# Optimization experiments

Measured on AMD Instinct MI355X. Metric: run time of the kernel, lower is better.

The kernel has to match this reference:

```python
import jax, jax.numpy as jnp
import numpy as np

TOP_K = 12
OBS_RADIUS = 1.0
DIST_MIN_THRES = 0.8
EPS = 1e-4


def setup_inputs() -> dict:
    key = jax.random.key(0)
    ks = jax.random.split(key, 9)
    N, in_dim = 4096, 4
    c = in_dim + 2  # pairwise diff + eye flag + (dist - thres)
    states = jax.random.normal(ks[0], (N, in_dim), dtype=jnp.float32) * 2.0
    def w(k, o, i):
        return jax.random.normal(k, (o, i), dtype=jnp.float32) * (1.0 / np.sqrt(i))
    return {
        "states": states,
        "W1": w(ks[1], 64, c),  "b1": jnp.zeros((64,), jnp.float32),
        "W2": w(ks[2], 128, 64), "b2": jnp.zeros((128,), jnp.float32),
        "W3": w(ks[3], 64, 128), "b3": jnp.zeros((64,), jnp.float32),
        "W4": w(ks[4], 1, 64),   "b4": jnp.zeros((1,), jnp.float32),
    }


def _conv1x1(h, W, b):
    # h: [N, C_in, L]; 1x1 Conv1d == channel matmul
    return jnp.einsum('oi,nil->nol', W, h) + b[None, :, None]


def reference(states, W1, b1, W2, b2, W3, b3, W4, b4):
    N = states.shape[0]
    # pairwise differences: [N, N, in_dim]
    x = states[:, None, :] - states[None, :, :]
    d_norm = jnp.sqrt(jnp.sum(jnp.square(x[:, :, :2]) + EPS, axis=2))  # [N, N]
    eye = jnp.eye(N, dtype=x.dtype)
    x = jnp.concatenate(
        [x, eye[:, :, None], (d_norm - DIST_MIN_THRES)[:, :, None]], axis=2
    )  # [N, N, c]
    # remove_distant_agents: keep TOP_K nearest neighbors per agent
    dn = jnp.sqrt(jnp.sum(jnp.square(x[:, :, :2]) + EPS, axis=2))  # [N, N]
    _, idx = jax.lax.top_k(-dn, TOP_K)                              # [N, k]
    x = jnp.take_along_axis(x, idx[:, :, None], axis=1)            # [N, k, c]
    dist = jnp.sqrt(jnp.sum(jnp.square(x[:, :, :2]) + EPS, axis=2, keepdims=True))  # [N,k,1]
    k, c = x.shape[1], x.shape[2]
    mask = (dist <= OBS_RADIUS).astype(x.dtype).reshape(-1, 1, k)  # [N,1,k] (reshape, as in source)
    h = x.reshape(-1, c, k)  # faithful: source uses reshape, NOT transpose
    h = jax.nn.relu(_conv1x1(h, W1, b1))
    h = jax.nn.relu(_conv1x1(h, W2, b2))
    h = jax.nn.relu(_conv1x1(h, W3, b3))
    h = _conv1x1(h, W4, b4)  # [N, 1, k]
    h = h * mask
    return h, mask
```

## Files before the change

### kernel.cpp

```cpp
#include <hip/hip_runtime.h>
#include <stdint.h>

#define NAG 4096
#define TOPK 12
#define EPSF 1e-4f
#define NT 512
#define WPB 8
#define NBLK (NAG / WPB)
#define MTOT (NAG * TOPK)

typedef unsigned long long u64;
typedef short short8v __attribute__((ext_vector_type(8)));
typedef float f32x4 __attribute__((ext_vector_type(4)));

__device__ __forceinline__ unsigned short f2bf(float f) {
    union { float f; unsigned u; } v; v.f = f;
    unsigned r = v.u + 0x7FFFu + ((v.u >> 16) & 1u);
    return (unsigned short)(r >> 16);
}

template <int CTRL>
__device__ __forceinline__ void dpp_min_step(unsigned &hi, unsigned &lo) {
    unsigned ohi = (unsigned)__builtin_amdgcn_update_dpp((int)hi, (int)hi, CTRL, 0xf, 0xf, false);
    unsigned olo = (unsigned)__builtin_amdgcn_update_dpp((int)lo, (int)lo, CTRL, 0xf, 0xf, false);
    bool t = (ohi < hi) || (ohi == hi && olo < lo);
    hi = t ? ohi : hi;
    lo = t ? olo : lo;
}

__global__ __launch_bounds__(256)
void cbf_prep(const float* __restrict__ W2, const float* __restrict__ W3,
              unsigned short* __restrict__ Wb) {
    int idx = blockIdx.x * 256 + threadIdx.x;
    float v = (idx < 8192) ? W2[idx] : W3[idx - 8192];
    Wb[idx] = f2bf(v);
}

__global__ __launch_bounds__(NT, 4)
void cbf_fused(const float* __restrict__ states,
               const float* __restrict__ W1, const float* __restrict__ b1,
               const unsigned short* __restrict__ Wb,
               const float* __restrict__ b2, const float* __restrict__ b3,
               const float* __restrict__ W4, const float* __restrict__ b4,
               float* __restrict__ out)
{
    const int t = threadIdx.x;
    const int lane = t & 63;
    const int wv = t >> 6;
    const int i = blockIdx.x * WPB + wv;

    __shared__ float2 s_xy[NAG];
    __shared__ u64 s_surv[WPB][64];
    __shared__ int s_sel[WPB][TOPK];
    __shared__ float s_x[WPB][72];
    __shared__ float s_mask[WPB][TOPK];
    __shared__ __align__(16) unsigned char s_h2[WPB][4096];

#pragma unroll
    for (int u = 0; u < 8; ++u) {
        int r = u * NT + t;
        float4 sr = reinterpret_cast<const float4*>(states)[r];
        s_xy[r] = make_float2(sr.x, sr.y);
    }
    __syncthreads();

    const float2 sif = s_xy[i];
    const float si0 = sif.x, si1 = sif.y;

    unsigned minb = 0xFFFFFFFFu;
    int minj = 0;
#pragma unroll 8
    for (int u = 0; u < 64; ++u) {
        float2 sj = s_xy[u * 64 + lane];
        float dx0 = __fsub_rn(si0, sj.x);
        float dx1 = __fsub_rn(si1, sj.y);
        float d2 = __fadd_rn(__fadd_rn(__fmul_rn(dx0, dx0), EPSF),
                             __fadd_rn(__fmul_rn(dx1, dx1), EPSF));
        unsigned b = __float_as_uint(__fsqrt_rn(d2));
        if (b < minb) { minb = b; minj = u * 64 + lane; }
    }

    unsigned Tb;
    {
        unsigned khi = minb, klo = (unsigned)minj;
        unsigned Tcur = 0;
        for (int r = 0; r < TOPK; ++r) {
            unsigned hi = khi, lo = klo;
            dpp_min_step<0xB1>(hi, lo);
            dpp_min_step<0x4E>(hi, lo);
            dpp_min_step<0x124>(hi, lo);
            dpp_min_step<0x128>(hi, lo);
            dpp_min_step<0x142>(hi, lo);
            dpp_min_step<0x143>(hi, lo);
            unsigned hw = (unsigned)__builtin_amdgcn_readlane((int)hi, 63);
            unsigned lw = (unsigned)__builtin_amdgcn_readlane((int)lo, 63);
            Tcur = hw;
            if (khi == hw && klo == lw) khi = 0xFFFFFFFFu;
        }
        Tb = Tcur;
    }

    int cnt = 0;
#pragma unroll 8
    for (int u = 0; u < 64; ++u) {
        float2 sj = s_xy[u * 64 + lane];
        float dx0 = __fsub_rn(si0, sj.x);
        float dx1 = __fsub_rn(si1, sj.y);
        float d2 = __fadd_rn(__fadd_rn(__fmul_rn(dx0, dx0), EPSF),
                             __fadd_rn(__fmul_rn(dx1, dx1), EPSF));
        unsigned b = __float_as_uint(__fsqrt_rn(d2));
        bool p = (b <= Tb);
        u64 mk = __ballot(p);
        if (p) {
            int pos = cnt + __popcll(mk & ((1ull << lane) - 1ull));
            if (pos < 64)
                s_surv[wv][pos] = ((u64)b << 32) | (unsigned)(u * 64 + lane);
        }
        cnt += __popcll(mk);
    }
    if (cnt > 64) cnt = 64;
    __asm volatile("s_waitcnt lgkmcnt(0)" ::: "memory");
    __builtin_amdgcn_wave_barrier();

    if (lane < cnt) {
        u64 kA = s_surv[wv][lane];
        int rA = 0;
        for (int q = 0; q < cnt; ++q)
            rA += (s_surv[wv][q] < kA) ? 1 : 0;
        if (rA < TOPK) s_sel[wv][rA] = (int)(unsigned)(kA & 0xffffffffull);
    }
    __asm volatile("s_waitcnt lgkmcnt(0)" ::: "memory");
    __builtin_amdgcn_wave_barrier();

    if (lane < TOPK) {
        int j = s_sel[wv][lane];
        const float4 sj = reinterpret_cast<const float4*>(states)[j];
        const float4 si = reinterpret_cast<const float4*>(states)[i];
        float dx0 = __fsub_rn(si.x, sj.x);
        float dx1 = __fsub_rn(si.y, sj.y);
        float dx2 = __fsub_rn(si.z, sj.z);
        float dx3 = __fsub_rn(si.w, sj.w);
        float d2 = __fadd_rn(__fadd_rn(__fmul_rn(dx0, dx0), EPSF),
                             __fadd_rn(__fmul_rn(dx1, dx1), EPSF));
        float dn = __fsqrt_rn(d2);
        s_x[wv][lane * 6 + 0] = dx0;
        s_x[wv][lane * 6 + 1] = dx1;
        s_x[wv][lane * 6 + 2] = dx2;
        s_x[wv][lane * 6 + 3] = dx3;
        s_x[wv][lane * 6 + 4] = (j == i) ? 1.0f : 0.0f;
        s_x[wv][lane * 6 + 5] = __fsub_rn(dn, 0.8f);
        float mk = (dn <= 1.0f) ? 1.0f : 0.0f;
        s_mask[wv][lane] = mk;
        out[MTOT + i * TOPK + lane] = mk;
    }
    __asm volatile("s_waitcnt lgkmcnt(0)" ::: "memory");
    __builtin_amdgcn_wave_barrier();

    const int r16 = lane & 15;
    const int hi = lane >> 4;

    float xc[6];
#pragma unroll
    for (int ch = 0; ch < 6; ++ch)
        xc[ch] = (r16 < TOPK) ? s_x[wv][ch * TOPK + r16] : 0.0f;

    short8v a0, a1;
#pragma unroll
    for (int e = 0; e < 8; ++e) {
        {
            int o = 8 * hi + e;
            const float2* wr = reinterpret_cast<const float2*>(W1 + o * 6);
            float2 w0 = wr[0], w1 = wr[1], w2 = wr[2];
            float acc = b1[o];
            acc = fmaf(w0.x, xc[0], acc);
            acc = fmaf(w0.y, xc[1], acc);
            acc = fmaf(w1.x, xc[2], acc);
            acc = fmaf(w1.y, xc[3], acc);
            acc = fmaf(w2.x, xc[4], acc);
            acc = fmaf(w2.y, xc[5], acc);
            a0[e] = (r16 < TOPK) ? (short)f2bf(fmaxf(acc, 0.0f)) : (short)0;
        }
        {
            int o = 32 + 8 * hi + e;
            const float2* wr = reinterpret_cast<const float2*>(W1 + o * 6);
            float2 w0 = wr[0], w1 = wr[1], w2 = wr[2];
            float acc = b1[o];
            acc = fmaf(w0.x, xc[0], acc);
            acc = fmaf(w0.y, xc[1], acc);
            acc = fmaf(w1.x, xc[2], acc);
            acc = fmaf(w1.y, xc[3], acc);
            acc = fmaf(w2.x, xc[4], acc);
            acc = fmaf(w2.y, xc[5], acc);
            a1[e] = (r16 < TOPK) ? (short)f2bf(fmaxf(acc, 0.0f)) : (short)0;
        }
    }

    unsigned char* lp2 = s_h2[wv];
    const int c = r16;

#pragma unroll
    for (int nt = 0; nt < 8; ++nt) {
        int o = nt * 16 + c;
        short8v bf0 = *(const short8v*)(Wb + o * 64 + 8 * hi);
        short8v bf1 = *(const short8v*)(Wb + o * 64 + 32 + 8 * hi);
        float bb = b2[o];
        f32x4 acc = {bb, bb, bb, bb};
        acc = __builtin_amdgcn_mfma_f32_16x16x32_bf16(a0, bf0, acc, 0, 0, 0);
        acc = __builtin_amdgcn_mfma_f32_16x16x32_bf16(a1, bf1, acc, 0, 0, 0);
#pragma unroll
        for (int e = 0; e < 4; ++e) {
            unsigned short hv = f2bf(fmaxf(acc[e], 0.0f));
            int mr = 4 * hi + e;
            int slot = (2 * nt + (c >> 3)) ^ (mr & 15);
            *(unsigned short*)(lp2 + mr * 256 + slot * 16 + ((2 * c) & 15)) = hv;
        }
    }
    __asm volatile("s_waitcnt lgkmcnt(0)" ::: "memory");
    __builtin_amdgcn_wave_barrier();

    short8v a3[4];
#pragma unroll
    for (int ks = 0; ks < 4; ++ks)
        a3[ks] = *(short8v*)(lp2 + r16 * 256 + (((4 * ks + hi) ^ r16) * 16));
    float h3r[4][4];
#pragma unroll
    for (int nt = 0; nt < 4; ++nt) {
        int o = nt * 16 + c;
        float bb = b3[o];
        f32x4 ac = {bb, bb, bb, bb};
#pragma unroll
        for (int ks = 0; ks < 4; ++ks) {
            short8v bf = *(const short8v*)(Wb + 8192 + o * 128 + ks * 32 + 8 * hi);
            ac = __builtin_amdgcn_mfma_f32_16x16x32_bf16(a3[ks], bf, ac, 0, 0, 0);
        }
#pragma unroll
        for (int e = 0; e < 4; ++e) h3r[nt][e] = fmaxf(ac[e], 0.0f);
    }

    float w4c[4];
#pragma unroll
    for (int nt = 0; nt < 4; ++nt) w4c[nt] = W4[nt * 16 + c];
    float part[4];
#pragma unroll
    for (int e = 0; e < 4; ++e) {
        float p = h3r[0][e] * w4c[0];
        p = fmaf(h3r[1][e], w4c[1], p);
        p = fmaf(h3r[2][e], w4c[2], p);
        p = fmaf(h3r[3][e], w4c[3], p);
        part[e] = p;
    }
#pragma unroll
    for (int off = 1; off <= 8; off <<= 1) {
#pragma unroll
        for (int e = 0; e < 4; ++e)
            part[e] += __shfl_xor(part[e], off, 64);
    }
    if (c == 0) {
        float bb4 = b4[0];
#pragma unroll
        for (int e = 0; e < 4; ++e) {
            int mr = 4 * hi + e;
            if (mr < TOPK)
                out[i * TOPK + mr] = (part[e] + bb4) * s_mask[wv][mr];
        }
    }
}

extern "C" void kernel_launch(void* const* d_in, const int* in_sizes, int n_in,
                              void* d_out, int out_size, void* d_ws, size_t ws_size,
                              hipStream_t stream) {
    const float* states = (const float*)d_in[0];
    const float* W1 = (const float*)d_in[1];
    const float* b1 = (const float*)d_in[2];
    const float* W2 = (const float*)d_in[3];
    const float* b2 = (const float*)d_in[4];
    const float* W3 = (const float*)d_in[5];
    const float* b3 = (const float*)d_in[6];
    const float* W4 = (const float*)d_in[7];
    const float* b4 = (const float*)d_in[8];
    float* out = (float*)d_out;
    unsigned short* Wb = (unsigned short*)d_ws;

    cbf_prep<<<dim3(64), dim3(256), 0, stream>>>(W2, W3, Wb);
    cbf_fused<<<dim3(NBLK), dim3(NT), 0, stream>>>(states, W1, b1, Wb,
                                                   b2, b3, W4, b4, out);
}
```

Measured before the change: 103.1 us.

## Split each agent's distance scan across two waves and halve the h2 staging buffer

Each agent is now handled by two waves, each scanning half of the 4096 candidates. The per-wave local minima are merged in shared memory for the top-k threshold search, and survivors are compacted through a shared atomic counter. Block size doubles to 1024 threads, and the second wave exits before the MLP stage. The layer-2/layer-3 MFMA chain is also reorganised into two halves so the bf16 h2 staging buffer shrinks from 4 KB to 2 KB per agent. The aim is to expose more parallelism in the scan, at the cost of extra block-wide barriers, atomics, and idle waves during the MLP.

```diff
diff --git a/kernel.cpp b/kernel.cpp
--- a/kernel.cpp
+++ b/kernel.cpp
@@ -4,9 +4,9 @@
 #define NAG 4096
 #define TOPK 12
 #define EPSF 1e-4f
-#define NT 512
-#define WPB 8
-#define NBLK (NAG / WPB)
+#define NT 1024
+#define APB 8
+#define NBLK (NAG / APB)
 #define MTOT (NAG * TOPK)
 
 typedef unsigned long long u64;
@@ -36,7 +36,7 @@
     Wb[idx] = f2bf(v);
 }
 
-__global__ __launch_bounds__(NT, 4)
+__global__ __launch_bounds__(NT, 8)
 void cbf_fused(const float* __restrict__ states,
                const float* __restrict__ W1, const float* __restrict__ b1,
                const unsigned short* __restrict__ Wb,
@@ -47,17 +47,24 @@
     const int t = threadIdx.x;
     const int lane = t & 63;
     const int wv = t >> 6;
-    const int i = blockIdx.x * WPB + wv;
+    const int a = wv >> 1;
+    const int p = wv & 1;
+    const int i = blockIdx.x * APB + a;
 
     __shared__ float2 s_xy[NAG];
-    __shared__ u64 s_surv[WPB][64];
-    __shared__ int s_sel[WPB][TOPK];
-    __shared__ float s_x[WPB][72];
-    __shared__ float s_mask[WPB][TOPK];
-    __shared__ __align__(16) unsigned char s_h2[WPB][4096];
-
-#pragma unroll
-    for (int u = 0; u < 8; ++u) {
+    __shared__ u64 s_lmin[APB][128];
+    __shared__ u64 s_surv[APB][64];
+    __shared__ int s_sel[APB][TOPK];
+    __shared__ float s_x[APB][72];
+    __shared__ float s_mask[APB][TOPK];
+    __shared__ unsigned s_cnt[APB];
+    __shared__ unsigned s_T[APB];
+    __shared__ __align__(16) unsigned char s_h2[APB][2048];
+
+    if (t < APB) s_cnt[t] = 0;
+
+#pragma unroll
+    for (int u = 0; u < 4; ++u) {
         int r = u * NT + t;
         float4 sr = reinterpret_cast<const float4*>(states)[r];
         s_xy[r] = make_float2(sr.x, sr.y);
@@ -70,22 +77,35 @@
     unsigned minb = 0xFFFFFFFFu;
     int minj = 0;
 #pragma unroll 8
-    for (int u = 0; u < 64; ++u) {
-        float2 sj = s_xy[u * 64 + lane];
+    for (int u = 0; u < 32; ++u) {
+        int j = (p * 32 + u) * 64 + lane;
+        float2 sj = s_xy[j];
         float dx0 = __fsub_rn(si0, sj.x);
         float dx1 = __fsub_rn(si1, sj.y);
         float d2 = __fadd_rn(__fadd_rn(__fmul_rn(dx0, dx0), EPSF),
                              __fadd_rn(__fmul_rn(dx1, dx1), EPSF));
         unsigned b = __float_as_uint(__fsqrt_rn(d2));
-        if (b < minb) { minb = b; minj = u * 64 + lane; }
-    }
-
-    unsigned Tb;
-    {
-        unsigned khi = minb, klo = (unsigned)minj;
-        unsigned Tcur = 0;
+        if (b < minb) { minb = b; minj = j; }
+    }
+    s_lmin[a][p * 64 + lane] = ((u64)minb << 32) | (unsigned)minj;
+    __syncthreads();
+
+    if (p == 0) {
+        unsigned khi[2], klo[2];
+#pragma unroll
+        for (int q = 0; q < 2; ++q) {
+            u64 kk = s_lmin[a][lane + q * 64];
+            klo[q] = (unsigned)(kk & 0xffffffffull);
+            khi[q] = (unsigned)(kk >> 32);
+        }
+        unsigned Tb = 0;
         for (int r = 0; r < TOPK; ++r) {
-            unsigned hi = khi, lo = klo;
+            unsigned hi = khi[0], lo = klo[0];
+            {
+                bool tk = (khi[1] < hi) || (khi[1] == hi && klo[1] < lo);
+                hi = tk ? khi[1] : hi;
+                lo = tk ? klo[1] : lo;
+            }
             dpp_min_step<0xB1>(hi, lo);
             dpp_min_step<0x4E>(hi, lo);
             dpp_min_step<0x124>(hi, lo);
@@ -94,46 +114,63 @@
             dpp_min_step<0x143>(hi, lo);
             unsigned hw = (unsigned)__builtin_amdgcn_readlane((int)hi, 63);
             unsigned lw = (unsigned)__builtin_amdgcn_readlane((int)lo, 63);
-            Tcur = hw;
-            if (khi == hw && klo == lw) khi = 0xFFFFFFFFu;
-        }
-        Tb = Tcur;
-    }
-
-    int cnt = 0;
+            Tb = hw;
+#pragma unroll
+            for (int q = 0; q < 2; ++q) {
+                bool w = (khi[q] == hw) && (klo[q] == lw);
+                khi[q] = w ? 0xFFFFFFFFu : khi[q];
+            }
+        }
+        if (lane == 0) s_T[a] = Tb;
+    }
+    __syncthreads();
+
+    {
+        unsigned Tb = s_T[a];
 #pragma unroll 8
-    for (int u = 0; u < 64; ++u) {
-        float2 sj = s_xy[u * 64 + lane];
-        float dx0 = __fsub_rn(si0, sj.x);
-        float dx1 = __fsub_rn(si1, sj.y);
-        float d2 = __fadd_rn(__fadd_rn(__fmul_rn(dx0, dx0), EPSF),
-                             __fadd_rn(__fmul_rn(dx1, dx1), EPSF));
-        unsigned b = __float_as_uint(__fsqrt_rn(d2));
-        bool p = (b <= Tb);
-        u64 mk = __ballot(p);
-        if (p) {
-            int pos = cnt + __popcll(mk & ((1ull << lane) - 1ull));
-            if (pos < 64)
-                s_surv[wv][pos] = ((u64)b << 32) | (unsigned)(u * 64 + lane);
-        }
-        cnt += __popcll(mk);
-    }
-    if (cnt > 64) cnt = 64;
+        for (int u = 0; u < 32; ++u) {
+            int j = (p * 32 + u) * 64 + lane;
+            float2 sj = s_xy[j];
+            float dx0 = __fsub_rn(si0, sj.x);
+            float dx1 = __fsub_rn(si1, sj.y);
+            float d2 = __fadd_rn(__fadd_rn(__fmul_rn(dx0, dx0), EPSF),
+                                 __fadd_rn(__fmul_rn(dx1, dx1), EPSF));
+            unsigned b = __float_as_uint(__fsqrt_rn(d2));
+            bool pr = (b <= Tb);
+            u64 mk = __ballot(pr);
+            if (mk != 0ull) {
+                unsigned nsel = (unsigned)__popcll(mk);
+                unsigned base = 0;
+                if (lane == 0) base = atomicAdd(&s_cnt[a], nsel);
+                base = (unsigned)__builtin_amdgcn_readfirstlane((int)base);
+                if (pr) {
+                    int pos = (int)base + __popcll(mk & ((1ull << lane) - 1ull));
+                    if (pos < 64)
+                        s_surv[a][pos] = ((u64)b << 32) | (unsigned)j;
+                }
+            }
+        }
+    }
+    __syncthreads();
+
+    if (p != 0) return;
+
+    {
+        int cnt = (int)s_cnt[a];
+        if (cnt > 64) cnt = 64;
+        if (lane < cnt) {
+            u64 kA = s_surv[a][lane];
+            int rA = 0;
+            for (int q = 0; q < cnt; ++q)
+                rA += (s_surv[a][q] < kA) ? 1 : 0;
+            if (rA < TOPK) s_sel[a][rA] = (int)(unsigned)(kA & 0xffffffffull);
+        }
+    }
     __asm volatile("s_waitcnt lgkmcnt(0)" ::: "memory");
     __builtin_amdgcn_wave_barrier();
 
-    if (lane < cnt) {
-        u64 kA = s_surv[wv][lane];
-        int rA = 0;
-        for (int q = 0; q < cnt; ++q)
-            rA += (s_surv[wv][q] < kA) ? 1 : 0;
-        if (rA < TOPK) s_sel[wv][rA] = (int)(unsigned)(kA & 0xffffffffull);
-    }
-    __asm volatile("s_waitcnt lgkmcnt(0)" ::: "memory");
-    __builtin_amdgcn_wave_barrier();
-
     if (lane < TOPK) {
-        int j = s_sel[wv][lane];
+        int j = s_sel[a][lane];
         const float4 sj = reinterpret_cast<const float4*>(states)[j];
         const float4 si = reinterpret_cast<const float4*>(states)[i];
         float dx0 = __fsub_rn(si.x, sj.x);
@@ -143,14 +180,14 @@
         float d2 = __fadd_rn(__fadd_rn(__fmul_rn(dx0, dx0), EPSF),
                              __fadd_rn(__fmul_rn(dx1, dx1), EPSF));
         float dn = __fsqrt_rn(d2);
-        s_x[wv][lane * 6 + 0] = dx0;
-        s_x[wv][lane * 6 + 1] = dx1;
-        s_x[wv][lane * 6 + 2] = dx2;
-        s_x[wv][lane * 6 + 3] = dx3;
-        s_x[wv][lane * 6 + 4] = (j == i) ? 1.0f : 0.0f;
-        s_x[wv][lane * 6 + 5] = __fsub_rn(dn, 0.8f);
+        s_x[a][lane * 6 + 0] = dx0;
+        s_x[a][lane * 6 + 1] = dx1;
+        s_x[a][lane * 6 + 2] = dx2;
+        s_x[a][lane * 6 + 3] = dx3;
+        s_x[a][lane * 6 + 4] = (j == i) ? 1.0f : 0.0f;
+        s_x[a][lane * 6 + 5] = __fsub_rn(dn, 0.8f);
         float mk = (dn <= 1.0f) ? 1.0f : 0.0f;
-        s_mask[wv][lane] = mk;
+        s_mask[a][lane] = mk;
         out[MTOT + i * TOPK + lane] = mk;
     }
     __asm volatile("s_waitcnt lgkmcnt(0)" ::: "memory");
@@ -158,11 +195,12 @@
 
     const int r16 = lane & 15;
     const int hi = lane >> 4;
+    const int c = r16;
 
     float xc[6];
 #pragma unroll
     for (int ch = 0; ch < 6; ++ch)
-        xc[ch] = (r16 < TOPK) ? s_x[wv][ch * TOPK + r16] : 0.0f;
+        xc[ch] = (r16 < TOPK) ? s_x[a][ch * TOPK + r16] : 0.0f;
 
     short8v a0, a1;
 #pragma unroll
@@ -195,47 +233,60 @@
         }
     }
 
-    unsigned char* lp2 = s_h2[wv];
-    const int c = r16;
-
-#pragma unroll
-    for (int nt = 0; nt < 8; ++nt) {
-        int o = nt * 16 + c;
-        short8v bf0 = *(const short8v*)(Wb + o * 64 + 8 * hi);
-        short8v bf1 = *(const short8v*)(Wb + o * 64 + 32 + 8 * hi);
-        float bb = b2[o];
-        f32x4 acc = {bb, bb, bb, bb};
-        acc = __builtin_amdgcn_mfma_f32_16x16x32_bf16(a0, bf0, acc, 0, 0, 0);
-        acc = __builtin_amdgcn_mfma_f32_16x16x32_bf16(a1, bf1, acc, 0, 0, 0);
-#pragma unroll
-        for (int e = 0; e < 4; ++e) {
-            unsigned short hv = f2bf(fmaxf(acc[e], 0.0f));
-            int mr = 4 * hi + e;
-            int slot = (2 * nt + (c >> 3)) ^ (mr & 15);
-            *(unsigned short*)(lp2 + mr * 256 + slot * 16 + ((2 * c) & 15)) = hv;
-        }
-    }
-    __asm volatile("s_waitcnt lgkmcnt(0)" ::: "memory");
-    __builtin_amdgcn_wave_barrier();
-
-    short8v a3[4];
-#pragma unroll
-    for (int ks = 0; ks < 4; ++ks)
-        a3[ks] = *(short8v*)(lp2 + r16 * 256 + (((4 * ks + hi) ^ r16) * 16));
+    unsigned char* lp2 = s_h2[a];
+
+    f32x4 ac3[4];
+#pragma unroll
+    for (int nt = 0; nt < 4; ++nt) {
+        float bb = b3[nt * 16 + c];
+        ac3[nt] = (f32x4){bb, bb, bb, bb};
+    }
+
+#pragma unroll
+    for (int half = 0; half < 2; ++half) {
+#pragma unroll
+        for (int ntl = 0; ntl < 4; ++ntl) {
+            int nt = half * 4 + ntl;
+            int o = nt * 16 + c;
+            short8v bf0 = *(const short8v*)(Wb + o * 64 + 8 * hi);
+            short8v bf1 = *(const short8v*)(Wb + o * 64 + 32 + 8 * hi);
+            float bb = b2[o];
+            f32x4 acc = {bb, bb, bb, bb};
+            acc = __builtin_amdgcn_mfma_f32_16x16x32_bf16(a0, bf0, acc, 0, 0, 0);
+            acc = __builtin_amdgcn_mfma_f32_16x16x32_bf16(a1, bf1, acc, 0, 0, 0);
+#pragma unroll
+            for (int e = 0; e < 4; ++e) {
+                unsigned short hv = f2bf(fmaxf(acc[e], 0.0f));
+                int mr = 4 * hi + e;
+                int slot = (2 * ntl + (c >> 3)) ^ (mr & 7);
+                *(unsigned short*)(lp2 + mr * 128 + slot * 16 + ((2 * c) & 15)) = hv;
+            }
+        }
+        __asm volatile("s_waitcnt lgkmcnt(0)" ::: "memory");
+        __builtin_amdgcn_wave_barrier();
+
+#pragma unroll
+        for (int ksl = 0; ksl < 2; ++ksl) {
+            short8v a3 = *(short8v*)(lp2 + r16 * 128 + (((4 * ksl + hi) ^ (r16 & 7)) * 16));
+            int ks = half * 2 + ksl;
+#pragma unroll
+            for (int nt = 0; nt < 4; ++nt) {
+                int o = nt * 16 + c;
+                short8v bf = *(const short8v*)(Wb + 8192 + o * 128 + ks * 32 + 8 * hi);
+                ac3[nt] = __builtin_amdgcn_mfma_f32_16x16x32_bf16(a3, bf, ac3[nt], 0, 0, 0);
+            }
+        }
+        if (half == 0) {
+            __asm volatile("s_waitcnt lgkmcnt(0)" ::: "memory");
+            __builtin_amdgcn_wave_barrier();
+        }
+    }
+
     float h3r[4][4];
 #pragma unroll
-    for (int nt = 0; nt < 4; ++nt) {
-        int o = nt * 16 + c;
-        float bb = b3[o];
-        f32x4 ac = {bb, bb, bb, bb};
-#pragma unroll
-        for (int ks = 0; ks < 4; ++ks) {
-            short8v bf = *(const short8v*)(Wb + 8192 + o * 128 + ks * 32 + 8 * hi);
-            ac = __builtin_amdgcn_mfma_f32_16x16x32_bf16(a3[ks], bf, ac, 0, 0, 0);
-        }
-#pragma unroll
-        for (int e = 0; e < 4; ++e) h3r[nt][e] = fmaxf(ac[e], 0.0f);
-    }
+    for (int nt = 0; nt < 4; ++nt)
+#pragma unroll
+        for (int e = 0; e < 4; ++e) h3r[nt][e] = fmaxf(ac3[nt][e], 0.0f);
 
     float w4c[4];
 #pragma unroll
@@ -243,11 +294,11 @@
     float part[4];
 #pragma unroll
     for (int e = 0; e < 4; ++e) {
-        float p = h3r[0][e] * w4c[0];
-        p = fmaf(h3r[1][e], w4c[1], p);
-        p = fmaf(h3r[2][e], w4c[2], p);
-        p = fmaf(h3r[3][e], w4c[3], p);
-        part[e] = p;
+        float pp = h3r[0][e] * w4c[0];
+        pp = fmaf(h3r[1][e], w4c[1], pp);
+        pp = fmaf(h3r[2][e], w4c[2], pp);
+        pp = fmaf(h3r[3][e], w4c[3], pp);
+        part[e] = pp;
     }
 #pragma unroll
     for (int off = 1; off <= 8; off <<= 1) {
@@ -261,7 +312,7 @@
         for (int e = 0; e < 4; ++e) {
             int mr = 4 * hi + e;
             if (mr < TOPK)
-                out[i * TOPK + mr] = (part[e] + bb4) * s_mask[wv][mr];
+                out[i * TOPK + mr] = (part[e] + bb4) * s_mask[a][mr];
         }
     }
 }
```

Result: slower. 114.1 us (+10.8%).
